# Optimization experiments

Measured on AMD Instinct MI355X. Metric: run time of the kernel, lower is better.

Reference implementation:

```python
import jax, jax.numpy as jnp
import numpy as np

N = 4608      # total nodes (48 graphs x 96 nodes)
B = 48
NPG = 96
D = 512       # vec_dim
XD = 16       # x_dim
E = N * 32    # GAT edges
L = 6         # GAT layers


def _w(k, shape, fan_in):
    return jax.random.normal(k, shape, jnp.float32) * (1.0 / np.sqrt(fan_in))


def setup_inputs() -> dict:
    key = jax.random.key(0)
    ks = jax.random.split(key, 24)
    x = jax.random.normal(ks[0], (N, XD), jnp.float32)
    xyz = jax.random.normal(ks[1], (N, 3), jnp.float32)
    edge_index = jax.random.randint(ks[2], (2, E), 0, N, dtype=jnp.int32)
    ptr = (jnp.arange(B + 1) * NPG).astype(jnp.int32)
    # complete graph with replacement per segment (torch.combinations order: i<=j)
    i, j = np.triu_indices(NPG)
    offs = (np.arange(B) * NPG)[:, None]
    cloud_edge_index = jnp.asarray(
        np.stack([(i[None, :] + offs).reshape(-1), (j[None, :] + offs).reshape(-1)]),
        jnp.int32)
    return {
        'x': x, 'edge_index': edge_index, 'ptr': ptr, 'xyz': xyz,
        'cloud_edge_index': cloud_edge_index,
        'x_proj_w': _w(ks[3], (XD, D), XD), 'x_proj_b': jnp.zeros((D,), jnp.float32),
        'gat_wl': _w(ks[4], (L, D, D), D), 'gat_bl': jnp.zeros((L, D), jnp.float32),
        'gat_wr': _w(ks[5], (L, D, D), D), 'gat_br': jnp.zeros((L, D), jnp.float32),
        'gat_att': _w(ks[6], (L, D), D), 'gat_bias': jnp.zeros((L, D), jnp.float32),
        'gat_ln_g': jnp.ones((L - 1, D), jnp.float32), 'gat_ln_b': jnp.zeros((L - 1, D), jnp.float32),
        'cg_xyz_w': _w(ks[7], (3, D), 3),
        'cg_bn_g': jnp.ones((D,), jnp.float32), 'cg_bn_b': jnp.zeros((D,), jnp.float32),
        'cg_lin1_w': _w(ks[8], (D, D), D), 'cg_lin1_b': jnp.zeros((D,), jnp.float32),
        'cg_ln_g': jnp.ones((D,), jnp.float32), 'cg_ln_b': jnp.zeros((D,), jnp.float32),
        'lin_w': _w(ks[9], (D, D), D), 'lin_b': jnp.zeros((D,), jnp.float32),
        'bn_g': jnp.ones((D,), jnp.float32), 'bn_b': jnp.zeros((D,), jnp.float32),
    }


def _batchnorm(t, g, b):
    mu = t.mean(0)
    v = ((t - mu) ** 2).mean(0)
    return (t - mu) / jnp.sqrt(v + 1e-5) * g + b


def _forward(x, edge_index, cloud_edge_index, x_proj_w, x_proj_b, gat_wl, gat_bl,
             gat_wr, gat_br, gat_att, gat_bias, gat_ln_g, gat_ln_b, cg_xyz_w,
             cg_bn_g, cg_bn_b, cg_lin1_w, cg_lin1_b, cg_ln_g, cg_ln_b,
             lin_w, lin_b, bn_g, bn_b, xyz):
    n = x.shape[0]
    h = x @ x_proj_w + x_proj_b  # [N, D]
    # ---- GATv2 stack (heads=1, self-loops added, eval mode: no dropout) ----
    loops = jnp.arange(n, dtype=edge_index.dtype)
    ei = jnp.concatenate([edge_index, jnp.stack([loops, loops])], axis=1)
    src, dst = ei[0], ei[1]
    xg = h
    for l in range(L):
        xl = xg @ gat_wl[l] + gat_bl[l]
        xr = xg @ gat_wr[l] + gat_br[l]
        e = jax.nn.leaky_relu(xl[src] + xr[dst], 0.2) @ gat_att[l]  # [E+N]
        m = jax.ops.segment_max(e, dst, num_segments=n)
        ew = jnp.exp(e - m[dst])
        den = jax.ops.segment_sum(ew, dst, num_segments=n)
        alpha = ew / den[dst]
        out = jax.ops.segment_sum(alpha[:, None] * xl[src], dst, num_segments=n) + gat_bias[l]
        if l < L - 1:
            # PyG LayerNorm, mode='graph', batch=None: normalize over all elements
            mu = out.mean()
            sd = jnp.sqrt(((out - mu) ** 2).mean())
            out = (out - mu) / (sd + 1e-5) * gat_ln_g[l] + gat_ln_b[l]
            out = jax.nn.relu(out)
        xg = out
    # ---- CloudGraph (complete graph gather-compute-scatter) ----
    a, b = cloud_edge_index[0], cloud_edge_index[1]
    rx = h[a] - h[b]          # [Ec, D]
    rz = xyz[a] - xyz[b]      # [Ec, 3]
    sq = (rz ** 2).sum(-1)
    dist = jnp.where(sq > 0, jnp.sqrt(jnp.where(sq > 0, sq, 1.0)), 0.0)
    w = jnp.exp(-dist)[:, None]
    p1 = jax.ops.segment_sum(jax.nn.relu((w * rx) @ cg_lin1_w + cg_lin1_b), a, num_segments=n)
    mu1 = p1.mean(-1, keepdims=True)
    v1 = ((p1 - mu1) ** 2).mean(-1, keepdims=True)
    ln1 = (p1 - mu1) / jnp.sqrt(v1 + 1e-5) * cg_ln_g + cg_ln_b
    p2 = jax.ops.segment_sum(jax.nn.relu(rz @ cg_xyz_w), a, num_segments=n)
    xc = h + ln1 + _batchnorm(p2, cg_bn_g, cg_bn_b)
    # ---- fuse + final norm ----
    return _batchnorm((h + xg + xc) @ lin_w + lin_b, bn_g, bn_b)


def reference(x, edge_index, ptr, xyz, cloud_edge_index, x_proj_w, x_proj_b,
              gat_wl, gat_bl, gat_wr, gat_br, gat_att, gat_bias, gat_ln_g,
              gat_ln_b, cg_xyz_w, cg_bn_g, cg_bn_b, cg_lin1_w, cg_lin1_b,
              cg_ln_g, cg_ln_b, lin_w, lin_b, bn_g, bn_b):
    return _forward(x, edge_index, cloud_edge_index, x_proj_w, x_proj_b, gat_wl,
                    gat_bl, gat_wr, gat_br, gat_att, gat_bias, gat_ln_g,
                    gat_ln_b, cg_xyz_w, cg_bn_g, cg_bn_b, cg_lin1_w, cg_lin1_b,
                    cg_ln_g, cg_ln_b, lin_w, lin_b, bn_g, bn_b, xyz)
```

## Files before the change

### kernel.cpp

```cpp
#include <hip/hip_runtime.h>
#include <hip/hip_bf16.h>

#define NN 4608
#define BG 48
#define NPG 96
#define DD 512
#define XDIM 16
#define EREAL 147456
#define NLAYER 6
#define NK 262144
#define TRIU 4656

typedef __hip_bfloat16 bf16;
typedef short short8 __attribute__((ext_vector_type(8)));
typedef short short4v __attribute__((ext_vector_type(4)));
typedef float f32x4 __attribute__((ext_vector_type(4)));

__device__ __forceinline__ float s2f(short s) {
  return __uint_as_float(((unsigned int)(unsigned short)s) << 16);
}
__device__ __forceinline__ short f2bs(float f) {
  bf16 h = __float2bfloat16(f);
  short s;
  __builtin_memcpy(&s, &h, 2);
  return s;
}

__global__ __launch_bounds__(256) void k_wt(const float* __restrict__ wl,
                                            const float* __restrict__ wr,
                                            const float* __restrict__ cg,
                                            const float* __restrict__ lin,
                                            bf16* __restrict__ Wt,
                                            int* __restrict__ counts,
                                            float* __restrict__ statsAll) {
  if (blockIdx.z == 0) {
    int id = (blockIdx.y * 16 + blockIdx.x) * 256 + threadIdx.x;
    if (id < NN) counts[id] = 0;
    if (id < 5 * 32) statsAll[id] = 0.f;
  }
  __shared__ float tile[32][33];
  int z = blockIdx.z;
  const float* src = (z < 6) ? wl + (size_t)z * NK
                   : (z < 12) ? wr + (size_t)(z - 6) * NK
                   : (z == 12) ? cg : lin;
  bf16* dst = Wt + (size_t)z * NK;
  int c = threadIdx.x & 31;
  int r0 = threadIdx.x >> 5;
  int bx = blockIdx.x * 32, by = blockIdx.y * 32;
#pragma unroll
  for (int i = 0; i < 4; i++) {
    int r = r0 + i * 8;
    tile[r][c] = src[(size_t)(by + r) * 512 + bx + c];
  }
  __syncthreads();
#pragma unroll
  for (int i = 0; i < 4; i++) {
    int r = r0 + i * 8;
    dst[(size_t)(bx + r) * 512 + by + c] = __float2bfloat16(tile[c][r]);
  }
}

__global__ void k_xproj(const float* __restrict__ x, const float* __restrict__ w,
                        const float* __restrict__ b, const int* __restrict__ ei,
                        const float* __restrict__ xyz, float* __restrict__ h,
                        bf16* __restrict__ h_bf, int* __restrict__ counts,
                        float* __restrict__ ep) {
  int i = blockIdx.x * blockDim.x + threadIdx.x;
  if (i >= NN * DD) return;
  if (i < EREAL) atomicAdd(&counts[ei[EREAL + i]], 1);
  if (i < NN * NPG) {
    int n = i / NPG, e = i - n * NPG;
    int p = n % NPG;
    if (e < NPG - p) {
      int g = n / NPG;
      int slot = g * TRIU + p * NPG - (p * (p - 1)) / 2 + e;
      int j = n + e;
      float dx = xyz[n * 3] - xyz[j * 3];
      float dy = xyz[n * 3 + 1] - xyz[j * 3 + 1];
      float dz = xyz[n * 3 + 2] - xyz[j * 3 + 2];
      float sq = dx * dx + dy * dy + dz * dz;
      float dist = (sq > 0.f) ? sqrtf(sq) : 0.f;
      float4 v;
      v.x = dx; v.y = dy; v.z = dz; v.w = __expf(-dist);
      *(float4*)&ep[(size_t)slot * 4] = v;
    }
  }
  int n = i >> 9, d = i & 511;
  float acc = b[d];
#pragma unroll
  for (int k = 0; k < XDIM; k++) acc += x[n * XDIM + k] * w[k * DD + d];
  h[i] = acc;
  h_bf[i] = __float2bfloat16(acc);
}

__global__ void k_scan(const int* __restrict__ counts, int* offsets, int* cursor) {
  __shared__ int part[256];
  __shared__ int pre[256];
  int t = threadIdx.x;
  int base = t * 18;
  int s = 0;
#pragma unroll
  for (int i = 0; i < 18; i++) s += counts[base + i];
  part[t] = s;
  __syncthreads();
  if (t == 0) {
    int r = 0;
    for (int i = 0; i < 256; i++) { pre[i] = r; r += part[i]; }
  }
  __syncthreads();
  int run = pre[t];
#pragma unroll
  for (int i = 0; i < 18; i++) {
    offsets[base + i] = run;
    cursor[base + i] = run;
    run += counts[base + i];
  }
  if (t == 0) offsets[NN] = EREAL;
}
__global__ void k_scatter(const int* __restrict__ ei, int* cursor, int* ssrc) {
  int e = blockIdx.x * blockDim.x + threadIdx.x;
  if (e < EREAL) {
    int s = ei[e], d = ei[EREAL + e];
    int pos = atomicAdd(&cursor[d], 1);
    ssrc[pos] = s;
  }
}

__global__ __launch_bounds__(256) void k_gemm(
    const float* __restrict__ Afp, const bf16* __restrict__ Abf,
    const bf16* __restrict__ B0, const bf16* __restrict__ B1,
    const float* __restrict__ bias0, const float* __restrict__ bias1,
    float* __restrict__ C0, float* __restrict__ C1,
    bf16* __restrict__ Cb0, bf16* __restrict__ Cb1,
    const float* __restrict__ statsIn,
    const float* __restrict__ lng, const float* __restrict__ lnb,
    float* __restrict__ zptr, int zn) {
  if (zptr && blockIdx.x == 0 && blockIdx.y == 0 && blockIdx.z == 0) {
    for (int i = threadIdx.x; i < zn; i += 256) zptr[i] = 0.f;
  }
  __shared__ __align__(16) bf16 As[128 * 40];
  __shared__ __align__(16) bf16 Bs[64 * 40];
  const bf16* B = blockIdx.z ? B1 : B0;
  const float* bias = blockIdx.z ? bias1 : bias0;
  float* C = blockIdx.z ? C1 : C0;
  bf16* Cb = blockIdx.z ? Cb1 : Cb0;
  int tid = threadIdx.x;
  int m0 = blockIdx.x * 128, n0 = blockIdx.y * 64;
  int lane = tid & 63, wid = tid >> 6;
  int mh = (wid >> 1) * 64, nh = (wid & 1) * 32;
  int l15 = lane & 15, quad = lane >> 4;

  float mu = 0.f, inv = 1.f;
  if (statsIn) {
    float s = 0.f, ss = 0.f;
#pragma unroll
    for (int i = 0; i < 16; i++) { s += statsIn[i]; ss += statsIn[16 + i]; }
    const float invM = 1.f / ((float)NN * (float)DD);
    mu = s * invM;
    float var = ss * invM - mu * mu;
    float sd = sqrtf(fmaxf(var, 0.f));
    inv = 1.f / (sd + 1e-5f);
  }

  f32x4 acc[4][2];
#pragma unroll
  for (int mt = 0; mt < 4; mt++)
#pragma unroll
    for (int nt = 0; nt < 2; nt++) acc[mt][nt] = (f32x4)0.f;

  for (int k0 = 0; k0 < 512; k0 += 32) {
    if (statsIn) {
#pragma unroll
      for (int it = 0; it < 2; it++) {
        int idx = tid + it * 256;
        int row = idx >> 2, kc = (idx & 3) * 8;
        const float* ap = &Afp[(size_t)(m0 + row) * 512 + k0 + kc];
        float4 va = *(const float4*)ap;
        float4 vb = *(const float4*)(ap + 4);
        float4 ga = *(const float4*)&lng[k0 + kc];
        float4 gb = *(const float4*)&lng[k0 + kc + 4];
        float4 ba = *(const float4*)&lnb[k0 + kc];
        float4 bb = *(const float4*)&lnb[k0 + kc + 4];
        float v[8] = {va.x, va.y, va.z, va.w, vb.x, vb.y, vb.z, vb.w};
        float gg[8] = {ga.x, ga.y, ga.z, ga.w, gb.x, gb.y, gb.z, gb.w};
        float bv[8] = {ba.x, ba.y, ba.z, ba.w, bb.x, bb.y, bb.z, bb.w};
        short8 pk;
#pragma unroll
        for (int k = 0; k < 8; k++) {
          float t = fmaxf((v[k] - mu) * inv * gg[k] + bv[k], 0.f);
          pk[k] = f2bs(t);
        }
        *(short8*)&As[row * 40 + kc] = pk;
      }
    } else {
#pragma unroll
      for (int it = 0; it < 2; it++) {
        int idx = tid + it * 256;
        int row = idx >> 2, kc = (idx & 3) * 8;
        *(short8*)&As[row * 40 + kc] =
            *(const short8*)&Abf[(size_t)(m0 + row) * 512 + k0 + kc];
      }
    }
    {
      int row = tid >> 2, kc = (tid & 3) * 8;
      *(short8*)&Bs[row * 40 + kc] =
          *(const short8*)&B[(size_t)(n0 + row) * 512 + k0 + kc];
    }
    __syncthreads();
    short8 af[4], bfr[2];
#pragma unroll
    for (int mt = 0; mt < 4; mt++)
      af[mt] = *(const short8*)&As[(mh + mt * 16 + l15) * 40 + quad * 8];
#pragma unroll
    for (int nt = 0; nt < 2; nt++)
      bfr[nt] = *(const short8*)&Bs[(nh + nt * 16 + l15) * 40 + quad * 8];
#pragma unroll
    for (int mt = 0; mt < 4; mt++)
#pragma unroll
      for (int nt = 0; nt < 2; nt++)
        acc[mt][nt] = __builtin_amdgcn_mfma_f32_16x16x32_bf16(
            af[mt], bfr[nt], acc[mt][nt], 0, 0, 0);
    __syncthreads();
  }
#pragma unroll
  for (int mt = 0; mt < 4; mt++) {
#pragma unroll
    for (int nt = 0; nt < 2; nt++) {
      int col = n0 + nh + nt * 16 + l15;
      float bv = bias ? bias[col] : 0.f;
#pragma unroll
      for (int r = 0; r < 4; r++) {
        int row = m0 + mh + mt * 16 + quad * 4 + r;
        float v = acc[mt][nt][r] + bv;
        if (C) C[(size_t)row * 512 + col] = v;
        if (Cb) Cb[(size_t)row * 512 + col] = __float2bfloat16(v);
      }
    }
  }
}

__global__ __launch_bounds__(256) void k_gat_edge(const bf16* __restrict__ xl,
                                                  const bf16* __restrict__ xr,
                                                  const float* __restrict__ att,
                                                  const float* __restrict__ bias,
                                                  const int* __restrict__ offs,
                                                  const int* __restrict__ ssrc,
                                                  float* __restrict__ out,
                                                  float* __restrict__ statsOut) {
  __shared__ float redS[4], redSS[4];
  int wave = (blockIdx.x * blockDim.x + threadIdx.x) >> 6;
  int lane = threadIdx.x & 63;
  int wid = threadIdx.x >> 6;
  if (wave < NN) {
    int n = wave;
    int base = lane * 8;
    float xrv[8], attv[8], acc[8];
    short8 xr8 = *(const short8*)&xr[(size_t)n * 512 + base];
#pragma unroll
    for (int k = 0; k < 8; k++) {
      xrv[k] = s2f(xr8[k]);
      attv[k] = att[base + k];
    }
    float m0, lsum;
    {
      short8 a8 = *(const short8*)&xl[(size_t)n * 512 + base];
      float sc0 = 0.f;
      float xs[8];
#pragma unroll
      for (int k = 0; k < 8; k++) {
        float v = s2f(a8[k]);
        xs[k] = v;
        float t = v + xrv[k];
        t = (t > 0.f) ? t : 0.2f * t;
        sc0 += attv[k] * t;
      }
#pragma unroll
      for (int off = 32; off >= 1; off >>= 1) sc0 += __shfl_xor(sc0, off, 64);
      m0 = sc0;
      lsum = 1.f;
#pragma unroll
      for (int k = 0; k < 8; k++) acc[k] = xs[k];
    }
    int e0 = offs[n], e1 = offs[n + 1];
    int e = e0;
    for (; e + 3 < e1; e += 4) {
      int s0 = ssrc[e], s1 = ssrc[e + 1], s2 = ssrc[e + 2], s3 = ssrc[e + 3];
      short8 a0 = *(const short8*)&xl[(size_t)s0 * 512 + base];
      short8 a1 = *(const short8*)&xl[(size_t)s1 * 512 + base];
      short8 a2 = *(const short8*)&xl[(size_t)s2 * 512 + base];
      short8 a3 = *(const short8*)&xl[(size_t)s3 * 512 + base];
      float x0[8], x1[8], x2[8], x3[8];
      float c0 = 0.f, c1 = 0.f, c2 = 0.f, c3 = 0.f;
#pragma unroll
      for (int k = 0; k < 8; k++) {
        float v0 = s2f(a0[k]), v1 = s2f(a1[k]), v2 = s2f(a2[k]), v3 = s2f(a3[k]);
        x0[k] = v0; x1[k] = v1; x2[k] = v2; x3[k] = v3;
        float t0 = v0 + xrv[k]; t0 = (t0 > 0.f) ? t0 : 0.2f * t0; c0 += attv[k] * t0;
        float t1 = v1 + xrv[k]; t1 = (t1 > 0.f) ? t1 : 0.2f * t1; c1 += attv[k] * t1;
        float t2 = v2 + xrv[k]; t2 = (t2 > 0.f) ? t2 : 0.2f * t2; c2 += attv[k] * t2;
        float t3 = v3 + xrv[k]; t3 = (t3 > 0.f) ? t3 : 0.2f * t3; c3 += attv[k] * t3;
      }
#pragma unroll
      for (int off = 32; off >= 1; off >>= 1) {
        c0 += __shfl_xor(c0, off, 64);
        c1 += __shfl_xor(c1, off, 64);
        c2 += __shfl_xor(c2, off, 64);
        c3 += __shfl_xor(c3, off, 64);
      }
      float p0 = __expf(c0 - m0), p1 = __expf(c1 - m0);
      float p2 = __expf(c2 - m0), p3 = __expf(c3 - m0);
      lsum += p0 + p1 + p2 + p3;
#pragma unroll
      for (int k = 0; k < 8; k++)
        acc[k] += p0 * x0[k] + p1 * x1[k] + p2 * x2[k] + p3 * x3[k];
    }
    for (; e < e1; ++e) {
      int s0 = ssrc[e];
      short8 a8 = *(const short8*)&xl[(size_t)s0 * 512 + base];
      float x0[8];
      float sc0 = 0.f;
#pragma unroll
      for (int k = 0; k < 8; k++) {
        float v0 = s2f(a8[k]);
        x0[k] = v0;
        float t0 = v0 + xrv[k];
        t0 = (t0 > 0.f) ? t0 : 0.2f * t0;
        sc0 += attv[k] * t0;
      }
#pragma unroll
      for (int off = 32; off >= 1; off >>= 1) sc0 += __shfl_xor(sc0, off, 64);
      float p0 = __expf(sc0 - m0);
      lsum += p0;
#pragma unroll
      for (int k = 0; k < 8; k++) acc[k] += p0 * x0[k];
    }
    float inv = 1.f / lsum;
    float o[8];
    float s = 0.f, ss = 0.f;
#pragma unroll
    for (int k = 0; k < 8; k++) {
      o[k] = acc[k] * inv + bias[base + k];
      s += o[k];
      ss += o[k] * o[k];
    }
    float4 st0, st1;
    st0.x = o[0]; st0.y = o[1]; st0.z = o[2]; st0.w = o[3];
    st1.x = o[4]; st1.y = o[5]; st1.z = o[6]; st1.w = o[7];
    *(float4*)&out[(size_t)n * 512 + base] = st0;
    *(float4*)&out[(size_t)n * 512 + base + 4] = st1;
    if (statsOut) {
#pragma unroll
      for (int off = 32; off >= 1; off >>= 1) {
        s += __shfl_xor(s, off, 64);
        ss += __shfl_xor(ss, off, 64);
      }
      if (lane == 0) { redS[wid] = s; redSS[wid] = ss; }
    }
  }
  if (statsOut) {
    __syncthreads();
    if (threadIdx.x == 0) {
      float a = redS[0] + redS[1] + redS[2] + redS[3];
      float b = redSS[0] + redSS[1] + redSS[2] + redSS[3];
      int slot = blockIdx.x & 15;
      atomicAdd(&statsOut[slot], a);
      atomicAdd(&statsOut[16 + slot], b);
    }
  }
}

__global__ __launch_bounds__(256) void k_cloud(const bf16* __restrict__ g1,
                                               const float* __restrict__ ep,
                                               const float* __restrict__ lin1b,
                                               const float* __restrict__ w3,
                                               float* __restrict__ p1,
                                               float* __restrict__ p2) {
  int w = (blockIdx.x * blockDim.x + threadIdx.x) >> 6;
  int lane = threadIdx.x & 63;
  if (w >= NN) return;
  int hf = w & 1;
  int pi = w >> 1;
  int g = pi / 48, pp = pi % 48;
  int d0 = hf * 256 + lane * 4;
  float4 bb = *(const float4*)&lin1b[d0];
  float4 w30 = *(const float4*)&w3[d0];
  float4 w31 = *(const float4*)&w3[512 + d0];
  float4 w32 = *(const float4*)&w3[1024 + d0];
  float bbv[4] = {bb.x, bb.y, bb.z, bb.w};
  float w0v[4] = {w30.x, w30.y, w30.z, w30.w};
  float w1v[4] = {w31.x, w31.y, w31.z, w31.w};
  float w2v[4] = {w32.x, w32.y, w32.z, w32.w};

#pragma unroll
  for (int half = 0; half < 2; half++) {
    int p = half ? (NPG - 1 - pp) : pp;
    int n = g * NPG + p;
    int cnt = NPG - p;
    int slot0 = g * TRIU + p * NPG - (p * (p - 1)) / 2;
    float gi[4], a1[4], a2[4];
    short4v gi4 = *(const short4v*)&g1[(size_t)n * 512 + d0];
#pragma unroll
    for (int k = 0; k < 4; k++) {
      gi[k] = s2f(gi4[k]);
      a1[k] = 0.f;
      a2[k] = 0.f;
    }
    int e = 0;
    for (; e + 1 < cnt; e += 2) {
      float4 pa = *(const float4*)&ep[(size_t)(slot0 + e) * 4];
      float4 pb = *(const float4*)&ep[(size_t)(slot0 + e + 1) * 4];
      short4v ga = *(const short4v*)&g1[(size_t)(n + e) * 512 + d0];
      short4v gb = *(const short4v*)&g1[(size_t)(n + e + 1) * 512 + d0];
#pragma unroll
      for (int k = 0; k < 4; k++) {
        float t = fmaf(pa.w, gi[k] - s2f(ga[k]), bbv[k]);
        a1[k] += fmaxf(t, 0.f);
        float u = fmaf(pb.w, gi[k] - s2f(gb[k]), bbv[k]);
        a1[k] += fmaxf(u, 0.f);
        float t2 = pa.x * w0v[k] + pa.y * w1v[k] + pa.z * w2v[k];
        a2[k] += fmaxf(t2, 0.f);
        float u2 = pb.x * w0v[k] + pb.y * w1v[k] + pb.z * w2v[k];
        a2[k] += fmaxf(u2, 0.f);
      }
    }
    if (e < cnt) {
      float4 pa = *(const float4*)&ep[(size_t)(slot0 + e) * 4];
      short4v ga = *(const short4v*)&g1[(size_t)(n + e) * 512 + d0];
#pragma unroll
      for (int k = 0; k < 4; k++) {
        float t = fmaf(pa.w, gi[k] - s2f(ga[k]), bbv[k]);
        a1[k] += fmaxf(t, 0.f);
        float t2 = pa.x * w0v[k] + pa.y * w1v[k] + pa.z * w2v[k];
        a2[k] += fmaxf(t2, 0.f);
      }
    }
    float4 o1, o2;
    o1.x = a1[0]; o1.y = a1[1]; o1.z = a1[2]; o1.w = a1[3];
    o2.x = a2[0]; o2.y = a2[1]; o2.z = a2[2]; o2.w = a2[3];
    *(float4*)&p1[(size_t)n * 512 + d0] = o1;
    *(float4*)&p2[(size_t)n * 512 + d0] = o2;
  }
}

__global__ __launch_bounds__(256) void k_cloud_epi(
    const float* __restrict__ p1, const float* __restrict__ p2,
    const float* __restrict__ h, const float* __restrict__ xg,
    const float* __restrict__ colsum, const float* __restrict__ colsq,
    const float* __restrict__ lng, const float* __restrict__ lnb,
    const float* __restrict__ bng, const float* __restrict__ bnb,
    bf16* __restrict__ s_bf) {
  int wave = (blockIdx.x * blockDim.x + threadIdx.x) >> 6;
  int lane = threadIdx.x & 63;
  if (wave >= NN) return;
  int n = wave;
  size_t rb = (size_t)n * 512 + lane * 8;
  int base = lane * 8;
  float v[8];
  float s = 0.f;
#pragma unroll
  for (int k = 0; k < 8; k++) {
    v[k] = p1[rb + k];
    s += v[k];
  }
#pragma unroll
  for (int off = 32; off >= 1; off >>= 1) s += __shfl_xor(s, off, 64);
  float mu = s * (1.f / 512.f);
  float ss = 0.f;
#pragma unroll
  for (int k = 0; k < 8; k++) {
    float t = v[k] - mu;
    ss += t * t;
  }
#pragma unroll
  for (int off = 32; off >= 1; off >>= 1) ss += __shfl_xor(ss, off, 64);
  float inv = 1.f / sqrtf(ss * (1.f / 512.f) + 1e-5f);
#pragma unroll
  for (int k = 0; k < 8; k++) {
    int d = base + k;
    float ln1 = (v[k] - mu) * inv * lng[d] + lnb[d];
    float cmu = colsum[d] * (1.f / NN);
    float cvar = colsq[d] * (1.f / NN) - cmu * cmu;
    float cinv = 1.f / sqrtf(fmaxf(cvar, 0.f) + 1e-5f);
    float bnv = (p2[rb + k] - cmu) * cinv * bng[d] + bnb[d];
    float out = 2.f * h[rb + k] + xg[rb + k] + ln1 + bnv;
    s_bf[rb + k] = __float2bfloat16(out);
  }
}

__global__ void k_col_reduce(const float* __restrict__ x, float* colsum, float* colsq) {
  int r0 = blockIdx.x * 128;
  int c0 = threadIdx.x;
  float s0 = 0.f, q0 = 0.f, s1 = 0.f, q1 = 0.f;
  for (int r = r0; r < r0 + 128; ++r) {
    float v = x[(size_t)r * 512 + c0];
    s0 += v;
    q0 += v * v;
    float w = x[(size_t)r * 512 + c0 + 256];
    s1 += w;
    q1 += w * w;
  }
  atomicAdd(&colsum[c0], s0);
  atomicAdd(&colsq[c0], q0);
  atomicAdd(&colsum[c0 + 256], s1);
  atomicAdd(&colsq[c0 + 256], q1);
}
__global__ void k_bn_out(const float* __restrict__ y, const float* __restrict__ colsum,
                         const float* __restrict__ colsq, const float* __restrict__ g,
                         const float* __restrict__ b, float* __restrict__ out) {
  int i = blockIdx.x * blockDim.x + threadIdx.x;
  if (i >= NN * DD) return;
  int d = i & 511;
  float mu = colsum[d] * (1.f / NN);
  float var = colsq[d] * (1.f / NN) - mu * mu;
  float inv = 1.f / sqrtf(fmaxf(var, 0.f) + 1e-5f);
  out[i] = (y[i] - mu) * inv * g[d] + b[d];
}

extern "C" void kernel_launch(void* const* d_in, const int* in_sizes, int n_in,
                              void* d_out, int out_size, void* d_ws, size_t ws_size,
                              hipStream_t stream) {
  const float* x = (const float*)d_in[0];
  const int* ei = (const int*)d_in[1];
  const float* xyz = (const float*)d_in[3];
  const float* x_proj_w = (const float*)d_in[5];
  const float* x_proj_b = (const float*)d_in[6];
  const float* gat_wl = (const float*)d_in[7];
  const float* gat_bl = (const float*)d_in[8];
  const float* gat_wr = (const float*)d_in[9];
  const float* gat_br = (const float*)d_in[10];
  const float* gat_att = (const float*)d_in[11];
  const float* gat_bias = (const float*)d_in[12];
  const float* gat_ln_g = (const float*)d_in[13];
  const float* gat_ln_b = (const float*)d_in[14];
  const float* cg_xyz_w = (const float*)d_in[15];
  const float* cg_bn_g = (const float*)d_in[16];
  const float* cg_bn_b = (const float*)d_in[17];
  const float* cg_lin1_w = (const float*)d_in[18];
  const float* cg_lin1_b = (const float*)d_in[19];
  const float* cg_ln_g = (const float*)d_in[20];
  const float* cg_ln_b = (const float*)d_in[21];
  const float* lin_w = (const float*)d_in[22];
  const float* lin_b = (const float*)d_in[23];
  const float* bn_g = (const float*)d_in[24];
  const float* bn_b = (const float*)d_in[25];

  const size_t ND = (size_t)NN * DD;
  char* w = (char*)d_ws;
  float* h = (float*)w;        w += ND * 4;
  float* xg = (float*)w;       w += ND * 4;
  float* p1 = (float*)w;       w += ND * 4;
  float* p2 = (float*)w;       w += ND * 4;
  bf16* h_bf = (bf16*)w;       w += ND * 2;
  bf16* xl_bf = (bf16*)w;      w += ND * 2;
  bf16* xr_bf = (bf16*)w;      w += ND * 2;
  bf16* Wt = (bf16*)w;         w += (size_t)14 * NK * 2;
  float* eparam = (float*)w;   w += (size_t)BG * TRIU * 16;
  int* counts = (int*)w;       w += NN * 4;
  int* offs = (int*)w;         w += (NN + 4) * 4;
  int* cursor = (int*)w;       w += NN * 4;
  int* ssrc = (int*)w;         w += EREAL * 4;
  float* statsAll = (float*)w; w += 5 * 32 * 4;
  float* colsum = (float*)w;   w += 512 * 4;
  float* colsq = (float*)w;    w += 512 * 4;
  float* y = p1;
  bf16* g1_bf = xl_bf;
  bf16* s_bf = h_bf;

  const int TPB = 256;
  const int ND_BLK = (int)((ND + TPB - 1) / TPB);

  k_wt<<<dim3(16, 16, 14), TPB, 0, stream>>>(gat_wl, gat_wr, cg_lin1_w, lin_w, Wt,
                                             counts, statsAll);
  k_xproj<<<ND_BLK, TPB, 0, stream>>>(x, x_proj_w, x_proj_b, ei, xyz, h, h_bf,
                                      counts, eparam);
  k_scan<<<1, 256, 0, stream>>>(counts, offs, cursor);
  k_scatter<<<(EREAL + TPB - 1) / TPB, TPB, 0, stream>>>(ei, cursor, ssrc);

  for (int l = 0; l < NLAYER; l++) {
    const float* sIn = (l > 0) ? statsAll + 32 * (l - 1) : nullptr;
    const float* lg = (l > 0) ? gat_ln_g + (l - 1) * DD : nullptr;
    const float* lb = (l > 0) ? gat_ln_b + (l - 1) * DD : nullptr;
    k_gemm<<<dim3(36, 8, 2), TPB, 0, stream>>>(
        xg, h_bf, Wt + (size_t)l * NK, Wt + (size_t)(6 + l) * NK,
        gat_bl + l * DD, gat_br + l * DD, nullptr, nullptr, xl_bf, xr_bf,
        sIn, lg, lb, nullptr, 0);
    float* sOut = (l < NLAYER - 1) ? statsAll + 32 * l : nullptr;
    k_gat_edge<<<NN / 4, TPB, 0, stream>>>(xl_bf, xr_bf, gat_att + l * DD,
                                           gat_bias + l * DD, offs, ssrc, xg, sOut);
  }

  k_gemm<<<dim3(36, 8, 1), TPB, 0, stream>>>(
      nullptr, h_bf, Wt + (size_t)12 * NK, Wt + (size_t)12 * NK, nullptr, nullptr,
      nullptr, nullptr, g1_bf, g1_bf, nullptr, nullptr, nullptr, colsum, 1024);
  k_cloud<<<NN / 4, TPB, 0, stream>>>(g1_bf, eparam, cg_lin1_b, cg_xyz_w, p1, p2);
  k_col_reduce<<<36, 256, 0, stream>>>(p2, colsum, colsq);
  k_cloud_epi<<<NN / 4, TPB, 0, stream>>>(p1, p2, h, xg, colsum, colsq,
                                          cg_ln_g, cg_ln_b, cg_bn_g, cg_bn_b, s_bf);

  k_gemm<<<dim3(36, 8, 1), TPB, 0, stream>>>(
      nullptr, s_bf, Wt + (size_t)13 * NK, Wt + (size_t)13 * NK, lin_b, lin_b,
      y, y, nullptr, nullptr, nullptr, nullptr, nullptr, colsum, 1024);
  k_col_reduce<<<36, 256, 0, stream>>>(y, colsum, colsq);
  k_bn_out<<<ND_BLK, TPB, 0, stream>>>(y, colsum, colsq, bn_g, bn_b, (float*)d_out);
}
```

Measured before the change: 617.8 us.

## Store GAT activations and h in bf16 and fuse final column stats into GEMM

Removes the fp32 copies of h and xg. The GAT edge kernel now writes bf16 output, and the next layer's LayerNorm prologue and the cloud epilogue read bf16. The final GEMM also accumulates per-column sum and sum-of-squares into shared memory and then global atomics, so the separate column-reduce kernel is dropped, and the cloud epilogue zeroes the new stat buffers. This cuts global memory traffic and one launch, at the cost of extra bf16 rounding on the intermediate activations and atomic contention.

```diff
diff --git a/kernel.cpp b/kernel.cpp
--- a/kernel.cpp
+++ b/kernel.cpp
@@ -62,7 +62,7 @@
 
 __global__ void k_xproj(const float* __restrict__ x, const float* __restrict__ w,
                         const float* __restrict__ b, const int* __restrict__ ei,
-                        const float* __restrict__ xyz, float* __restrict__ h,
+                        const float* __restrict__ xyz,
                         bf16* __restrict__ h_bf, int* __restrict__ counts,
                         float* __restrict__ ep) {
   int i = blockIdx.x * blockDim.x + threadIdx.x;
@@ -89,7 +89,6 @@
   float acc = b[d];
 #pragma unroll
   for (int k = 0; k < XDIM; k++) acc += x[n * XDIM + k] * w[k * DD + d];
-  h[i] = acc;
   h_bf[i] = __float2bfloat16(acc);
 }
 
@@ -127,19 +126,21 @@
 }
 
 __global__ __launch_bounds__(256) void k_gemm(
-    const float* __restrict__ Afp, const bf16* __restrict__ Abf,
+    const bf16* __restrict__ Abf,
     const bf16* __restrict__ B0, const bf16* __restrict__ B1,
     const float* __restrict__ bias0, const float* __restrict__ bias1,
     float* __restrict__ C0, float* __restrict__ C1,
     bf16* __restrict__ Cb0, bf16* __restrict__ Cb1,
     const float* __restrict__ statsIn,
     const float* __restrict__ lng, const float* __restrict__ lnb,
-    float* __restrict__ zptr, int zn) {
+    float* __restrict__ zptr, int zn,
+    float* __restrict__ csum, float* __restrict__ csq) {
   if (zptr && blockIdx.x == 0 && blockIdx.y == 0 && blockIdx.z == 0) {
     for (int i = threadIdx.x; i < zn; i += 256) zptr[i] = 0.f;
   }
   __shared__ __align__(16) bf16 As[128 * 40];
   __shared__ __align__(16) bf16 Bs[64 * 40];
+  __shared__ float cs[64], cq[64];
   const bf16* B = blockIdx.z ? B1 : B0;
   const float* bias = blockIdx.z ? bias1 : bias0;
   float* C = blockIdx.z ? C1 : C0;
@@ -150,6 +151,8 @@
   int mh = (wid >> 1) * 64, nh = (wid & 1) * 32;
   int l15 = lane & 15, quad = lane >> 4;
 
+  if (csum && tid < 64) { cs[tid] = 0.f; cq[tid] = 0.f; }
+
   float mu = 0.f, inv = 1.f;
   if (statsIn) {
     float s = 0.f, ss = 0.f;
@@ -174,20 +177,17 @@
       for (int it = 0; it < 2; it++) {
         int idx = tid + it * 256;
         int row = idx >> 2, kc = (idx & 3) * 8;
-        const float* ap = &Afp[(size_t)(m0 + row) * 512 + k0 + kc];
-        float4 va = *(const float4*)ap;
-        float4 vb = *(const float4*)(ap + 4);
+        short8 raw = *(const short8*)&Abf[(size_t)(m0 + row) * 512 + k0 + kc];
         float4 ga = *(const float4*)&lng[k0 + kc];
         float4 gb = *(const float4*)&lng[k0 + kc + 4];
         float4 ba = *(const float4*)&lnb[k0 + kc];
         float4 bb = *(const float4*)&lnb[k0 + kc + 4];
-        float v[8] = {va.x, va.y, va.z, va.w, vb.x, vb.y, vb.z, vb.w};
         float gg[8] = {ga.x, ga.y, ga.z, ga.w, gb.x, gb.y, gb.z, gb.w};
         float bv[8] = {ba.x, ba.y, ba.z, ba.w, bb.x, bb.y, bb.z, bb.w};
         short8 pk;
 #pragma unroll
         for (int k = 0; k < 8; k++) {
-          float t = fmaxf((v[k] - mu) * inv * gg[k] + bv[k], 0.f);
+          float t = fmaxf((s2f(raw[k]) - mu) * inv * gg[k] + bv[k], 0.f);
           pk[k] = f2bs(t);
         }
         *(short8*)&As[row * 40 + kc] = pk;
@@ -222,6 +222,7 @@
             af[mt], bfr[nt], acc[mt][nt], 0, 0, 0);
     __syncthreads();
   }
+  float colS[2] = {0.f, 0.f}, colQ[2] = {0.f, 0.f};
 #pragma unroll
   for (int mt = 0; mt < 4; mt++) {
 #pragma unroll
@@ -234,7 +235,20 @@
         float v = acc[mt][nt][r] + bv;
         if (C) C[(size_t)row * 512 + col] = v;
         if (Cb) Cb[(size_t)row * 512 + col] = __float2bfloat16(v);
-      }
+        if (csum) { colS[nt] += v; colQ[nt] += v * v; }
+      }
+    }
+  }
+  if (csum) {
+#pragma unroll
+    for (int nt = 0; nt < 2; nt++) {
+      atomicAdd(&cs[nh + nt * 16 + l15], colS[nt]);
+      atomicAdd(&cq[nh + nt * 16 + l15], colQ[nt]);
+    }
+    __syncthreads();
+    if (tid < 64) {
+      atomicAdd(&csum[n0 + tid], cs[tid]);
+      atomicAdd(&csq[n0 + tid], cq[tid]);
     }
   }
 }
@@ -245,7 +259,7 @@
                                                   const float* __restrict__ bias,
                                                   const int* __restrict__ offs,
                                                   const int* __restrict__ ssrc,
-                                                  float* __restrict__ out,
+                                                  bf16* __restrict__ out,
                                                   float* __restrict__ statsOut) {
   __shared__ float redS[4], redSS[4];
   int wave = (blockIdx.x * blockDim.x + threadIdx.x) >> 6;
@@ -265,11 +279,10 @@
     {
       short8 a8 = *(const short8*)&xl[(size_t)n * 512 + base];
       float sc0 = 0.f;
-      float xs[8];
 #pragma unroll
       for (int k = 0; k < 8; k++) {
         float v = s2f(a8[k]);
-        xs[k] = v;
+        acc[k] = v;
         float t = v + xrv[k];
         t = (t > 0.f) ? t : 0.2f * t;
         sc0 += attv[k] * t;
@@ -278,8 +291,6 @@
       for (int off = 32; off >= 1; off >>= 1) sc0 += __shfl_xor(sc0, off, 64);
       m0 = sc0;
       lsum = 1.f;
-#pragma unroll
-      for (int k = 0; k < 8; k++) acc[k] = xs[k];
     }
     int e0 = offs[n], e1 = offs[n + 1];
     int e = e0;
@@ -337,17 +348,15 @@
     float inv = 1.f / lsum;
     float o[8];
     float s = 0.f, ss = 0.f;
+    short8 o8;
 #pragma unroll
     for (int k = 0; k < 8; k++) {
       o[k] = acc[k] * inv + bias[base + k];
       s += o[k];
       ss += o[k] * o[k];
-    }
-    float4 st0, st1;
-    st0.x = o[0]; st0.y = o[1]; st0.z = o[2]; st0.w = o[3];
-    st1.x = o[4]; st1.y = o[5]; st1.z = o[6]; st1.w = o[7];
-    *(float4*)&out[(size_t)n * 512 + base] = st0;
-    *(float4*)&out[(size_t)n * 512 + base + 4] = st1;
+      o8[k] = f2bs(o[k]);
+    }
+    *(short8*)&out[(size_t)n * 512 + base] = o8;
     if (statsOut) {
 #pragma unroll
       for (int off = 32; off >= 1; off >>= 1) {
@@ -444,11 +453,14 @@
 
 __global__ __launch_bounds__(256) void k_cloud_epi(
     const float* __restrict__ p1, const float* __restrict__ p2,
-    const float* __restrict__ h, const float* __restrict__ xg,
+    const bf16* __restrict__ h_bf, const bf16* __restrict__ xg_bf,
     const float* __restrict__ colsum, const float* __restrict__ colsq,
     const float* __restrict__ lng, const float* __restrict__ lnb,
     const float* __restrict__ bng, const float* __restrict__ bnb,
-    bf16* __restrict__ s_bf) {
+    bf16* __restrict__ s_bf, float* __restrict__ zptr) {
+  if (blockIdx.x == 0) {
+    for (int i = threadIdx.x; i < 1024; i += 256) zptr[i] = 0.f;
+  }
   int wave = (blockIdx.x * blockDim.x + threadIdx.x) >> 6;
   int lane = threadIdx.x & 63;
   if (wave >= NN) return;
@@ -474,6 +486,9 @@
 #pragma unroll
   for (int off = 32; off >= 1; off >>= 1) ss += __shfl_xor(ss, off, 64);
   float inv = 1.f / sqrtf(ss * (1.f / 512.f) + 1e-5f);
+  short8 hb = *(const short8*)&h_bf[rb];
+  short8 xb = *(const short8*)&xg_bf[rb];
+  short8 o8;
 #pragma unroll
   for (int k = 0; k < 8; k++) {
     int d = base + k;
@@ -482,9 +497,10 @@
     float cvar = colsq[d] * (1.f / NN) - cmu * cmu;
     float cinv = 1.f / sqrtf(fmaxf(cvar, 0.f) + 1e-5f);
     float bnv = (p2[rb + k] - cmu) * cinv * bng[d] + bnb[d];
-    float out = 2.f * h[rb + k] + xg[rb + k] + ln1 + bnv;
-    s_bf[rb + k] = __float2bfloat16(out);
-  }
+    float out = 2.f * s2f(hb[k]) + s2f(xb[k]) + ln1 + bnv;
+    o8[k] = f2bs(out);
+  }
+  *(short8*)&s_bf[rb] = o8;
 }
 
 __global__ void k_col_reduce(const float* __restrict__ x, float* colsum, float* colsq) {
@@ -546,11 +562,10 @@
 
   const size_t ND = (size_t)NN * DD;
   char* w = (char*)d_ws;
-  float* h = (float*)w;        w += ND * 4;
-  float* xg = (float*)w;       w += ND * 4;
   float* p1 = (float*)w;       w += ND * 4;
   float* p2 = (float*)w;       w += ND * 4;
   bf16* h_bf = (bf16*)w;       w += ND * 2;
+  bf16* xg_bf = (bf16*)w;      w += ND * 2;
   bf16* xl_bf = (bf16*)w;      w += ND * 2;
   bf16* xr_bf = (bf16*)w;      w += ND * 2;
   bf16* Wt = (bf16*)w;         w += (size_t)14 * NK * 2;
@@ -562,6 +577,8 @@
   float* statsAll = (float*)w; w += 5 * 32 * 4;
   float* colsum = (float*)w;   w += 512 * 4;
   float* colsq = (float*)w;    w += 512 * 4;
+  float* colsum2 = (float*)w;  w += 512 * 4;
+  float* colsq2 = (float*)w;   w += 512 * 4;
   float* y = p1;
   bf16* g1_bf = xl_bf;
   bf16* s_bf = h_bf;
@@ -571,35 +588,40 @@
 
   k_wt<<<dim3(16, 16, 14), TPB, 0, stream>>>(gat_wl, gat_wr, cg_lin1_w, lin_w, Wt,
                                              counts, statsAll);
-  k_xproj<<<ND_BLK, TPB, 0, stream>>>(x, x_proj_w, x_proj_b, ei, xyz, h, h_bf,
+  k_xproj<<<ND_BLK, TPB, 0, stream>>>(x, x_proj_w, x_proj_b, ei, xyz, h_bf,
                                       counts, eparam);
   k_scan<<<1, 256, 0, stream>>>(counts, offs, cursor);
   k_scatter<<<(EREAL + TPB - 1) / TPB, TPB, 0, stream>>>(ei, cursor, ssrc);
 
   for (int l = 0; l < NLAYER; l++) {
+    const bf16* A = (l == 0) ? h_bf : xg_bf;
     const float* sIn = (l > 0) ? statsAll + 32 * (l - 1) : nullptr;
     const float* lg = (l > 0) ? gat_ln_g + (l - 1) * DD : nullptr;
     const float* lb = (l > 0) ? gat_ln_b + (l - 1) * DD : nullptr;
     k_gemm<<<dim3(36, 8, 2), TPB, 0, stream>>>(
-        xg, h_bf, Wt + (size_t)l * NK, Wt + (size_t)(6 + l) * NK,
+        A, Wt + (size_t)l * NK, Wt + (size_t)(6 + l) * NK,
         gat_bl + l * DD, gat_br + l * DD, nullptr, nullptr, xl_bf, xr_bf,
-        sIn, lg, lb, nullptr, 0);
+        sIn, lg, lb, nullptr, 0, nullptr, nullptr);
     float* sOut = (l < NLAYER - 1) ? statsAll + 32 * l : nullptr;
     k_gat_edge<<<NN / 4, TPB, 0, stream>>>(xl_bf, xr_bf, gat_att + l * DD,
-                                           gat_bias + l * DD, offs, ssrc, xg, sOut);
+                                           gat_bias + l * DD, offs, ssrc,
+                                           xg_bf, sOut);
   }
 
   k_gemm<<<dim3(36, 8, 1), TPB, 0, stream>>>(
-      nullptr, h_bf, Wt + (size_t)12 * NK, Wt + (size_t)12 * NK, nullptr, nullptr,
-      nullptr, nullptr, g1_bf, g1_bf, nullptr, nullptr, nullptr, colsum, 1024);
+      h_bf, Wt + (size_t)12 * NK, Wt + (size_t)12 * NK, nullptr, nullptr,
+      nullptr, nullptr, g1_bf, g1_bf, nullptr, nullptr, nullptr,
+      colsum, 1024, nullptr, nullptr);
   k_cloud<<<NN / 4, TPB, 0, stream>>>(g1_bf, eparam, cg_lin1_b, cg_xyz_w, p1, p2);
   k_col_reduce<<<36, 256, 0, stream>>>(p2, colsum, colsq);
-  k_cloud_epi<<<NN / 4, TPB, 0, stream>>>(p1, p2, h, xg, colsum, colsq,
-                                          cg_ln_g, cg_ln_b, cg_bn_g, cg_bn_b, s_bf);
+  k_cloud_epi<<<NN / 4, TPB, 0, stream>>>(p1, p2, h_bf, xg_bf, colsum, colsq,
+                                          cg_ln_g, cg_ln_b, cg_bn_g, cg_bn_b,
+                                          s_bf, colsum2);
 
   k_gemm<<<dim3(36, 8, 1), TPB, 0, stream>>>(
-      nullptr, s_bf, Wt + (size_t)13 * NK, Wt + (size_t)13 * NK, lin_b, lin_b,
-      y, y, nullptr, nullptr, nullptr, nullptr, nullptr, colsum, 1024);
-  k_col_reduce<<<36, 256, 0, stream>>>(y, colsum, colsq);
-  k_bn_out<<<ND_BLK, TPB, 0, stream>>>(y, colsum, colsq, bn_g, bn_b, (float*)d_out);
-}
+      s_bf, Wt + (size_t)13 * NK, Wt + (size_t)13 * NK, lin_b, lin_b,
+      y, y, nullptr, nullptr, nullptr, nullptr, nullptr,
+      nullptr, 0, colsum2, colsq2);
+  k_bn_out<<<ND_BLK, TPB, 0, stream>>>(y, colsum2, colsq2, bn_g, bn_b,
+                                       (float*)d_out);
+}
```

New measurement: 598.7 us. 3.1% less time.
